# Kernel optimization log

Hardware: AMD Instinct MI355X
Metric: run time of the kernel (lower is better)

The kernel has to match this reference:

```python
import jax, jax.numpy as jnp
import numpy as np

B, N, C = 2, 120000, 80
K = 300            # fixed NMS candidate pad per class (>> expected ~150 above threshold)
MAX_DET = 100      # max_detections_per_images
SCORE_THRES = 0.99875
NMS_THRES = 0.5
MIN_SIZE = 1e-3    # remove_small_boxes min_size
BBOX_CLIP = float(np.log(1000.0 / 16.0))  # standard decode clamp on dw, dh


def _decode(deltas, anchors):
    # activ_2_bbox: standard anchor-delta decode (xyxy anchors)
    wa = anchors[:, 2] - anchors[:, 0]
    ha = anchors[:, 3] - anchors[:, 1]
    cxa = anchors[:, 0] + 0.5 * wa
    cya = anchors[:, 1] + 0.5 * ha
    dx, dy = deltas[:, 0], deltas[:, 1]
    dw = jnp.minimum(deltas[:, 2], BBOX_CLIP)
    dh = jnp.minimum(deltas[:, 3], BBOX_CLIP)
    cx = dx * wa + cxa
    cy = dy * ha + cya
    w = jnp.exp(dw) * wa
    h = jnp.exp(dh) * ha
    return jnp.stack([cx - 0.5 * w, cy - 0.5 * h, cx + 0.5 * w, cy + 0.5 * h], axis=-1)


def _pairwise_iou(b):
    area = (b[:, 2] - b[:, 0]) * (b[:, 3] - b[:, 1])
    lt = jnp.maximum(b[:, None, :2], b[None, :, :2])
    rb = jnp.minimum(b[:, None, 2:], b[None, :, 2:])
    wh = jnp.clip(rb - lt, 0.0)
    inter = wh[..., 0] * wh[..., 1]
    return inter / (area[:, None] + area[None, :] - inter + 1e-9)


def _nms_keep(boxes, valid):
    # boxes sorted by descending score; greedy suppression over K candidates
    iou = jax.lax.stop_gradient(_pairwise_iou(boxes))  # masks only -> no grad path
    idx = jnp.arange(boxes.shape[0])
    def body(keep, i):
        suppress = keep[i] & (iou[i] > NMS_THRES) & (idx > i)
        return keep & ~suppress, None
    keep, _ = jax.lax.scan(body, valid, idx)
    return keep


def _per_image(box_pred, cls_pred, anchors, H, W):
    boxes = _decode(box_pred, anchors)
    boxes = jnp.stack([
        jnp.clip(boxes[:, 0], 0.0, W), jnp.clip(boxes[:, 1], 0.0, H),
        jnp.clip(boxes[:, 2], 0.0, W), jnp.clip(boxes[:, 3], 0.0, H)], axis=-1)
    big = ((boxes[:, 2] - boxes[:, 0]) >= MIN_SIZE) & ((boxes[:, 3] - boxes[:, 1]) >= MIN_SIZE)

    def class_step(valid, c):
        # faithful to the original: the validity set carries over across classes
        sc = cls_pred[:, c]
        v = valid & big & (sc > SCORE_THRES)
        ms = jnp.where(v, sc, -jnp.inf)
        sk, idx = jax.lax.top_k(ms, K)            # sorted desc, fixed-size pad
        vk = sk > -jnp.inf
        bk = boxes[idx]                            # [K,4]
        keep = _nms_keep(bk, vk)
        keep = keep & ((jnp.cumsum(keep) - 1) < MAX_DET)  # keep[:max_det]
        new_valid = jnp.zeros_like(valid).at[idx].set(keep)
        bk = jnp.where(keep[:, None], bk, 0.0)
        sk = jnp.where(keep, sk, 0.0)
        return new_valid, (bk, sk, keep)

    _, (bks, sks, keeps) = jax.lax.scan(class_step, jnp.ones(boxes.shape[0], bool), jnp.arange(C))
    out5 = jnp.concatenate([bks, sks[..., None]], axis=-1).reshape(C * K, 5)
    labels = jnp.broadcast_to(jnp.arange(C, dtype=jnp.int32)[:, None], (C, K)).reshape(C * K)
    return out5, labels, keeps.reshape(C * K)


def setup_inputs() -> dict:
    key = jax.random.key(0)
    k1, k2, k3, k4, k5 = jax.random.split(key, 5)
    H, W = 800, 1216
    box_preds = 0.2 * jax.random.normal(k1, (B, N, 4), jnp.float32)
    cls_preds = jax.random.uniform(k2, (B, N, C), dtype=jnp.float32)
    cx = jax.random.uniform(k3, (N,), dtype=jnp.float32) * W
    cy = jax.random.uniform(k4, (N,), dtype=jnp.float32) * H
    wh = 16.0 + 240.0 * jax.random.uniform(k5, (N, 2), dtype=jnp.float32)
    anchors = jnp.stack([cx - 0.5 * wh[:, 0], cy - 0.5 * wh[:, 1],
                         cx + 0.5 * wh[:, 0], cy + 0.5 * wh[:, 1]], axis=-1)
    return {"box_preds": box_preds, "cls_preds": cls_preds, "anchors": anchors,
            "image_h": H, "image_w": W}


def reference(box_preds, cls_preds, anchors, image_h, image_w):
    H = jnp.float32(image_h)
    W = jnp.float32(image_w)
    out5, labels, keep = jax.vmap(lambda bp, cp: _per_image(bp, cp, anchors, H, W))(box_preds, cls_preds)
    # out5: [B, C*K, 5] (x1,y1,x2,y2,score), zero-padded where keep is False
    return out5, labels, keep
```

## Files before the change

### kernel.cpp

```cpp
#include <hip/hip_runtime.h>
#include <stdint.h>

#define B_ 2
#define N_ 120000
#define C_ 80
#define K_ 300
#define MAXDET 100
#define CAP 1024
#define KTOP 300
#define NW 5
#define NB 235
#define TPB 256
#define SLOTS 32

__device__ __constant__ float SCORE_THRES_F = 0.99875f;
__device__ __constant__ float NMS_THRES_F   = 0.5f;
__device__ __constant__ float MIN_SIZE_F    = 0.001f;
__device__ __constant__ float BBOX_CLIP_F   = 4.135166556742356f;

__global__ __launch_bounds__(TPB) void filter_init(
    const float* __restrict__ boxp, const float* __restrict__ clsp,
    const float* __restrict__ anch, const int* __restrict__ ih,
    const int* __restrict__ iw, int* __restrict__ cnt,
    int* __restrict__ g_idx, float* __restrict__ g_sc,
    float4* __restrict__ g_bx, float* __restrict__ out) {
#pragma clang fp contract(off)
    __shared__ int lcnt[2];
    const int blk = blockIdx.x;
    const int ltid = threadIdx.x;
    const int NT  = NB * TPB;
    const int tid = blk * TPB + ltid;
    if (ltid < 2) lcnt[ltid] = 0;

    const int BN = B_ * N_;
    float s[4]; int t4[4];
#pragma unroll
    for (int k = 0; k < 4; ++k) {
        int t = tid + k * NT;
        t4[k] = t;
        s[k] = (t < BN) ? clsp[(size_t)t * C_] : 0.f;
    }

    const int CK  = C_ * K_;
    const int L0  = B_ * CK * 5;
    const int L1  = L0 + B_ * CK;
    const int TOT = L1 + B_ * CK;
    for (int i = tid; i < TOT; i += NT) {
        float v = 0.f;
        if (i >= L0 && i < L1) { int r = i - L0; v = (float)((r % CK) / K_); }
        out[i] = v;
    }
    __syncthreads();

#pragma unroll
    for (int k = 0; k < 4; ++k) {
        int t = t4[k];
        if (t < BN && s[k] > SCORE_THRES_F) {
            int b = t / N_, n = t - b * N_;
            float W = (float)iw[0], H = (float)ih[0];
            float4 d = *(const float4*)(boxp + (size_t)t * 4);
            float4 a = *(const float4*)(anch + (size_t)n * 4);
            float wa = a.z - a.x, ha = a.w - a.y;
            float cxa = a.x + 0.5f * wa, cya = a.y + 0.5f * ha;
            float dw = fminf(d.z, BBOX_CLIP_F), dh = fminf(d.w, BBOX_CLIP_F);
            float cx = d.x * wa + cxa, cy = d.y * ha + cya;
            float w = expf(dw) * wa, h = expf(dh) * ha;
            float x1 = cx - 0.5f * w, y1 = cy - 0.5f * h;
            float x2 = cx + 0.5f * w, y2 = cy + 0.5f * h;
            x1 = fminf(fmaxf(x1, 0.f), W);
            y1 = fminf(fmaxf(y1, 0.f), H);
            x2 = fminf(fmaxf(x2, 0.f), W);
            y2 = fminf(fmaxf(y2, 0.f), H);
            if ((x2 - x1 >= MIN_SIZE_F) && (y2 - y1 >= MIN_SIZE_F)) {
                int p = atomicAdd(&lcnt[b], 1);
                if (p < SLOTS) {
                    int q = (b * NB + blk) * SLOTS + p;
                    g_idx[q] = n;
                    g_sc[q]  = s[k];
                    g_bx[q]  = make_float4(x1, y1, x2, y2);
                }
            }
        }
    }
    __syncthreads();
    if (ltid < 2) cnt[ltid * NB + blk] = min(lcnt[ltid], SLOTS);
}

__global__ __launch_bounds__(TPB) void seq_nms(const float* __restrict__ clsp,
                                               const int* __restrict__ cnt,
                                               const int* __restrict__ g_idx,
                                               const float* __restrict__ g_sc,
                                               const float4* __restrict__ g_bx,
                                               float* __restrict__ out) {
#pragma clang fp contract(off)
    const int b   = blockIdx.x;
    const int tid = threadIdx.x;
    const int BS  = blockDim.x;

    __shared__ __align__(16) float s_sc[CAP];
    __shared__ __align__(16) int   s_id[CAP];
    __shared__ float4 s_bx[CAP];
    __shared__ float  o_sc[KTOP];
    __shared__ int    o_id[KTOP];
    __shared__ float  o_ar[KTOP];
    __shared__ float  o_nsc[KTOP];
    __shared__ float4 o_bx[KTOP];
    __shared__ unsigned long long suppW[KTOP * NW];
    __shared__ unsigned long long keepm[NW];
    __shared__ int s_cnt, s_nk, s_m;
    __shared__ int wsum[4];
    __shared__ int    n_id[MAXDET];
    __shared__ float  n_sc[MAXDET];
    __shared__ float4 n_bx[MAXDET];

    if (tid == 0) s_nk = 0;
    const size_t CK = (size_t)C_ * K_;

    for (int c = 0; c < C_; ++c) {
        if (c > 0 && s_nk == 0) break;
        if (tid == 0) s_cnt = 0;
        __syncthreads();

        int m_in;
        if (c == 0) {
            int lane = tid & 63, wvi = tid >> 6;
            int v = (tid < NB) ? cnt[b * NB + tid] : 0;
            int x = v;
            for (int d = 1; d < 64; d <<= 1) {
                int y = __shfl_up(x, d);
                if (lane >= d) x += y;
            }
            if (lane == 63) wsum[wvi] = x;
            __syncthreads();
            int offbase = 0;
            for (int w = 0; w < wvi; ++w) offbase += wsum[w];
            if (tid == BS - 1) s_m = offbase + x;
            int excl = offbase + x - v;
            for (int j = 0; j < v; ++j) {
                int dst = excl + j;
                if (dst < CAP) {
                    int src = (b * NB + tid) * SLOTS + j;
                    s_sc[dst] = g_sc[src];
                    s_id[dst] = g_idx[src];
                    s_bx[dst] = g_bx[src];
                }
            }
            __syncthreads();
            m_in = min(s_m, CAP);
        } else {
            int nk = s_nk;
            for (int t = tid; t < nk; t += BS) {
                float sv = n_sc[t];
                if (sv > SCORE_THRES_F) {
                    int p = atomicAdd(&s_cnt, 1);
                    s_sc[p] = sv; s_id[p] = n_id[t]; s_bx[p] = n_bx[t];
                }
            }
            __syncthreads();
            m_in = s_cnt;
        }
        int m = min(m_in, KTOP);
        if (m == 0) {
            if (tid == 0) s_nk = 0;
            __syncthreads();
            continue;
        }

        for (int i = tid; i < m_in; i += BS) {
            float si = s_sc[i]; int di = s_id[i]; float4 bx = s_bx[i];
            float ns = 0.f;
            if (c + 1 < C_) ns = clsp[((size_t)(b * N_) + di) * C_ + (c + 1)];
            int rank = 0;
            int m4 = m_in & ~3;
            for (int j = 0; j < m4; j += 4) {
                float4 sj = *(const float4*)&s_sc[j];
                int4   dj = *(const int4*)&s_id[j];
                rank += (sj.x > si) || (sj.x == si && dj.x < di);
                rank += (sj.y > si) || (sj.y == si && dj.y < di);
                rank += (sj.z > si) || (sj.z == si && dj.z < di);
                rank += (sj.w > si) || (sj.w == si && dj.w < di);
            }
            for (int j = m4; j < m_in; ++j) {
                float sj = s_sc[j];
                rank += (sj > si) || (sj == si && s_id[j] < di);
            }
            if (rank < KTOP) {
                o_sc[rank] = si; o_id[rank] = di; o_bx[rank] = bx;
                o_ar[rank] = (bx.z - bx.x) * (bx.w - bx.y);
                o_nsc[rank] = ns;
            }
        }
        __syncthreads();

        for (int i = tid; i < m; i += BS) {
            float4 bi = o_bx[i]; float ai = o_ar[i];
            for (int w = 0; w < NW; ++w) {
                unsigned long long msk = 0ull;
                int jlo = max(i + 1, w * 64);
                int jhi = min(m, w * 64 + 64);
#pragma unroll 4
                for (int j = jlo; j < jhi; ++j) {
                    float4 bj = o_bx[j];
                    float lx = fmaxf(bi.x, bj.x), ly = fmaxf(bi.y, bj.y);
                    float rx = fminf(bi.z, bj.z), ry = fminf(bi.w, bj.w);
                    float ww = fmaxf(rx - lx, 0.f), hh = fmaxf(ry - ly, 0.f);
                    float inter = ww * hh;
                    float arj = (bj.z - bj.x) * (bj.w - bj.y);
                    float iou = inter / (ai + arj - inter + 1e-9f);
                    if (iou > NMS_THRES_F) msk |= 1ull << (j & 63);
                }
                suppW[i * NW + w] = msk;
            }
        }
        __syncthreads();

        if (tid < 64) {
            int lane = tid;
            unsigned long long km = 0ull;
            if (lane < NW) {
                int nb = m - lane * 64;
                if (nb >= 64) km = ~0ull;
                else if (nb > 0) km = (1ull << nb) - 1ull;
            }
            unsigned long long srow = (lane < NW) ? suppW[lane] : 0ull;
            for (int i = 0; i < m; ++i) {
                unsigned long long nxt =
                    (lane < NW && i + 1 < m) ? suppW[(i + 1) * NW + lane] : 0ull;
                unsigned long long wv = __shfl(km, i >> 6);
                if ((wv >> (i & 63)) & 1ull) km &= ~srow;
                srow = nxt;
            }
            unsigned long long w0 = __shfl(km, 0), w1 = __shfl(km, 1),
                               w2 = __shfl(km, 2), w3 = __shfl(km, 3),
                               w4 = __shfl(km, 4);
            if (lane == 0) {
                unsigned long long arr[NW] = {w0, w1, w2, w3, w4};
                int cnt2 = 0;
                for (int w = 0; w < NW; ++w) {
                    unsigned long long x = arr[w];
                    if (cnt2 >= MAXDET) { arr[w] = 0ull; continue; }
                    int pc = __popcll(x);
                    if (cnt2 + pc > MAXDET) {
                        int need = MAXDET - cnt2;
                        unsigned long long y = x;
                        for (int k2 = 0; k2 < need; ++k2) y &= y - 1ull;
                        arr[w] = x ^ y;
                        cnt2 = MAXDET;
                    } else cnt2 += pc;
                }
                int tot = 0;
                for (int w = 0; w < NW; ++w) { keepm[w] = arr[w]; tot += __popcll(arr[w]); }
                s_nk = tot;
            }
        }
        __syncthreads();

        for (int r = tid; r < m; r += BS) {
            unsigned long long wv = keepm[r >> 6];
            if ((wv >> (r & 63)) & 1ull) {
                int pos = __popcll(wv & ((1ull << (r & 63)) - 1ull));
                for (int w = 0; w < (r >> 6); ++w) pos += __popcll(keepm[w]);
                size_t row = (size_t)b * CK + (size_t)c * K_ + r;
                float4 bx = o_bx[r];
                float* o5 = out + row * 5;
                o5[0] = bx.x; o5[1] = bx.y; o5[2] = bx.z; o5[3] = bx.w;
                o5[4] = o_sc[r];
                out[(size_t)B_ * CK * 6 + row] = 1.0f;
                n_id[pos] = o_id[r];
                n_bx[pos] = bx;
                n_sc[pos] = o_nsc[r];
            }
        }
    }
}

extern "C" void kernel_launch(void* const* d_in, const int* in_sizes, int n_in,
                              void* d_out, int out_size, void* d_ws, size_t ws_size,
                              hipStream_t stream) {
    const float* boxp = (const float*)d_in[0];
    const float* clsp = (const float*)d_in[1];
    const float* anch = (const float*)d_in[2];
    const int*   ih   = (const int*)d_in[3];
    const int*   iw   = (const int*)d_in[4];
    float* out = (float*)d_out;

    int*    cnt   = (int*)d_ws;
    int*    g_idx = (int*)((char*)d_ws + 4096);
    float*  g_sc  = (float*)((char*)d_ws + 4096 + (size_t)B_ * NB * SLOTS * 4);
    float4* g_bx  = (float4*)((char*)d_ws + 4096 + (size_t)B_ * NB * SLOTS * 8);

    filter_init<<<NB, TPB, 0, stream>>>(boxp, clsp, anch, ih, iw,
                                        cnt, g_idx, g_sc, g_bx, out);
    seq_nms<<<B_, TPB, 0, stream>>>(clsp, cnt, g_idx, g_sc, g_bx, out);
}
```

Baseline: 149.8 us.

## Fuse filter and NMS into one cooperative kernel; bit-skip greedy NMS scan

Merges the filter/decode kernel and the per-image sequential NMS kernel into a single cooperative launch with a grid-wide sync, removing one kernel launch and the inter-kernel gap. The greedy suppression loop now preloads the suppression rows into registers and walks only the surviving candidate bits with ctz and readlane, instead of iterating over every candidate with shuffles. The cooperative launch needs all 237 blocks resident at once, and a grid sync has its own cost. The fused kernel also carries the large NMS shared-memory footprint in every block, which may limit occupancy during the filter phase.

```diff
diff --git a/kernel.cpp b/kernel.cpp
--- a/kernel.cpp
+++ b/kernel.cpp
@@ -1,5 +1,8 @@
 #include <hip/hip_runtime.h>
+#include <hip/hip_cooperative_groups.h>
 #include <stdint.h>
+
+namespace cg = cooperative_groups;
 
 #define B_ 2
 #define N_ 120000
@@ -18,85 +21,23 @@
 __device__ __constant__ float MIN_SIZE_F    = 0.001f;
 __device__ __constant__ float BBOX_CLIP_F   = 4.135166556742356f;
 
-__global__ __launch_bounds__(TPB) void filter_init(
+__device__ __forceinline__ unsigned long long rl64(unsigned long long v, int lane) {
+    unsigned lo = (unsigned)__builtin_amdgcn_readlane((int)(unsigned)(v & 0xffffffffull), lane);
+    unsigned hi = (unsigned)__builtin_amdgcn_readlane((int)(unsigned)(v >> 32), lane);
+    return ((unsigned long long)hi << 32) | lo;
+}
+
+__global__ __launch_bounds__(TPB) void retina_fused(
     const float* __restrict__ boxp, const float* __restrict__ clsp,
     const float* __restrict__ anch, const int* __restrict__ ih,
     const int* __restrict__ iw, int* __restrict__ cnt,
     int* __restrict__ g_idx, float* __restrict__ g_sc,
     float4* __restrict__ g_bx, float* __restrict__ out) {
 #pragma clang fp contract(off)
+    const int blk  = blockIdx.x;
+    const int ltid = threadIdx.x;
+
     __shared__ int lcnt[2];
-    const int blk = blockIdx.x;
-    const int ltid = threadIdx.x;
-    const int NT  = NB * TPB;
-    const int tid = blk * TPB + ltid;
-    if (ltid < 2) lcnt[ltid] = 0;
-
-    const int BN = B_ * N_;
-    float s[4]; int t4[4];
-#pragma unroll
-    for (int k = 0; k < 4; ++k) {
-        int t = tid + k * NT;
-        t4[k] = t;
-        s[k] = (t < BN) ? clsp[(size_t)t * C_] : 0.f;
-    }
-
-    const int CK  = C_ * K_;
-    const int L0  = B_ * CK * 5;
-    const int L1  = L0 + B_ * CK;
-    const int TOT = L1 + B_ * CK;
-    for (int i = tid; i < TOT; i += NT) {
-        float v = 0.f;
-        if (i >= L0 && i < L1) { int r = i - L0; v = (float)((r % CK) / K_); }
-        out[i] = v;
-    }
-    __syncthreads();
-
-#pragma unroll
-    for (int k = 0; k < 4; ++k) {
-        int t = t4[k];
-        if (t < BN && s[k] > SCORE_THRES_F) {
-            int b = t / N_, n = t - b * N_;
-            float W = (float)iw[0], H = (float)ih[0];
-            float4 d = *(const float4*)(boxp + (size_t)t * 4);
-            float4 a = *(const float4*)(anch + (size_t)n * 4);
-            float wa = a.z - a.x, ha = a.w - a.y;
-            float cxa = a.x + 0.5f * wa, cya = a.y + 0.5f * ha;
-            float dw = fminf(d.z, BBOX_CLIP_F), dh = fminf(d.w, BBOX_CLIP_F);
-            float cx = d.x * wa + cxa, cy = d.y * ha + cya;
-            float w = expf(dw) * wa, h = expf(dh) * ha;
-            float x1 = cx - 0.5f * w, y1 = cy - 0.5f * h;
-            float x2 = cx + 0.5f * w, y2 = cy + 0.5f * h;
-            x1 = fminf(fmaxf(x1, 0.f), W);
-            y1 = fminf(fmaxf(y1, 0.f), H);
-            x2 = fminf(fmaxf(x2, 0.f), W);
-            y2 = fminf(fmaxf(y2, 0.f), H);
-            if ((x2 - x1 >= MIN_SIZE_F) && (y2 - y1 >= MIN_SIZE_F)) {
-                int p = atomicAdd(&lcnt[b], 1);
-                if (p < SLOTS) {
-                    int q = (b * NB + blk) * SLOTS + p;
-                    g_idx[q] = n;
-                    g_sc[q]  = s[k];
-                    g_bx[q]  = make_float4(x1, y1, x2, y2);
-                }
-            }
-        }
-    }
-    __syncthreads();
-    if (ltid < 2) cnt[ltid * NB + blk] = min(lcnt[ltid], SLOTS);
-}
-
-__global__ __launch_bounds__(TPB) void seq_nms(const float* __restrict__ clsp,
-                                               const int* __restrict__ cnt,
-                                               const int* __restrict__ g_idx,
-                                               const float* __restrict__ g_sc,
-                                               const float4* __restrict__ g_bx,
-                                               float* __restrict__ out) {
-#pragma clang fp contract(off)
-    const int b   = blockIdx.x;
-    const int tid = threadIdx.x;
-    const int BS  = blockDim.x;
-
     __shared__ __align__(16) float s_sc[CAP];
     __shared__ __align__(16) int   s_id[CAP];
     __shared__ float4 s_bx[CAP];
@@ -112,6 +53,72 @@
     __shared__ int    n_id[MAXDET];
     __shared__ float  n_sc[MAXDET];
     __shared__ float4 n_bx[MAXDET];
+
+    if (blk < NB) {
+        const int NT  = NB * TPB;
+        const int tid = blk * TPB + ltid;
+        if (ltid < 2) lcnt[ltid] = 0;
+
+        const int BN = B_ * N_;
+        float s[4]; int t4[4];
+#pragma unroll
+        for (int k = 0; k < 4; ++k) {
+            int t = tid + k * NT;
+            t4[k] = t;
+            s[k] = (t < BN) ? clsp[(size_t)t * C_] : 0.f;
+        }
+
+        const int CK  = C_ * K_;
+        const int L0  = B_ * CK * 5;
+        const int L1  = L0 + B_ * CK;
+        const int TOT = L1 + B_ * CK;
+        for (int i = tid; i < TOT; i += NT) {
+            float v = 0.f;
+            if (i >= L0 && i < L1) { int r = i - L0; v = (float)((r % CK) / K_); }
+            out[i] = v;
+        }
+        __syncthreads();
+
+#pragma unroll
+        for (int k = 0; k < 4; ++k) {
+            int t = t4[k];
+            if (t < BN && s[k] > SCORE_THRES_F) {
+                int b = t / N_, n = t - b * N_;
+                float W = (float)iw[0], H = (float)ih[0];
+                float4 d = *(const float4*)(boxp + (size_t)t * 4);
+                float4 a = *(const float4*)(anch + (size_t)n * 4);
+                float wa = a.z - a.x, ha = a.w - a.y;
+                float cxa = a.x + 0.5f * wa, cya = a.y + 0.5f * ha;
+                float dw = fminf(d.z, BBOX_CLIP_F), dh = fminf(d.w, BBOX_CLIP_F);
+                float cx = d.x * wa + cxa, cy = d.y * ha + cya;
+                float w = expf(dw) * wa, h = expf(dh) * ha;
+                float x1 = cx - 0.5f * w, y1 = cy - 0.5f * h;
+                float x2 = cx + 0.5f * w, y2 = cy + 0.5f * h;
+                x1 = fminf(fmaxf(x1, 0.f), W);
+                y1 = fminf(fmaxf(y1, 0.f), H);
+                x2 = fminf(fmaxf(x2, 0.f), W);
+                y2 = fminf(fmaxf(y2, 0.f), H);
+                if ((x2 - x1 >= MIN_SIZE_F) && (y2 - y1 >= MIN_SIZE_F)) {
+                    int p = atomicAdd(&lcnt[b], 1);
+                    if (p < SLOTS) {
+                        int q = (b * NB + blk) * SLOTS + p;
+                        g_idx[q] = n;
+                        g_sc[q]  = s[k];
+                        g_bx[q]  = make_float4(x1, y1, x2, y2);
+                    }
+                }
+            }
+        }
+        __syncthreads();
+        if (ltid < 2) cnt[ltid * NB + blk] = min(lcnt[ltid], SLOTS);
+    }
+
+    cg::this_grid().sync();
+    if (blk < NB) return;
+
+    const int b   = blk - NB;
+    const int tid = ltid;
+    const int BS  = TPB;
 
     if (tid == 0) s_nk = 0;
     const size_t CK = (size_t)C_ * K_;
@@ -215,42 +222,50 @@
         __syncthreads();
 
         if (tid < 64) {
-            int lane = tid;
-            unsigned long long km = 0ull;
-            if (lane < NW) {
-                int nb = m - lane * 64;
-                if (nb >= 64) km = ~0ull;
-                else if (nb > 0) km = (1ull << nb) - 1ull;
-            }
-            unsigned long long srow = (lane < NW) ? suppW[lane] : 0ull;
-            for (int i = 0; i < m; ++i) {
-                unsigned long long nxt =
-                    (lane < NW && i + 1 < m) ? suppW[(i + 1) * NW + lane] : 0ull;
-                unsigned long long wv = __shfl(km, i >> 6);
-                if ((wv >> (i & 63)) & 1ull) km &= ~srow;
-                srow = nxt;
-            }
-            unsigned long long w0 = __shfl(km, 0), w1 = __shfl(km, 1),
-                               w2 = __shfl(km, 2), w3 = __shfl(km, 3),
-                               w4 = __shfl(km, 4);
+            const int lane = tid;
+            unsigned long long row[NW][NW];
+#pragma unroll
+            for (int g = 0; g < NW; ++g) {
+                int i = g * 64 + lane;
+#pragma unroll
+                for (int w = 0; w < NW; ++w)
+                    row[g][w] = (w >= g && i < m) ? suppW[i * NW + w] : 0ull;
+            }
+            unsigned long long km[NW];
+#pragma unroll
+            for (int w = 0; w < NW; ++w) {
+                int nb2 = m - w * 64;
+                km[w] = (nb2 >= 64) ? ~0ull : (nb2 > 0 ? ((1ull << nb2) - 1ull) : 0ull);
+            }
+#pragma unroll
+            for (int g = 0; g < NW; ++g) {
+                unsigned long long pend = km[g];
+                while (pend) {
+                    int t = __builtin_ctzll(pend);
+#pragma unroll
+                    for (int w = 0; w < NW; ++w)
+                        if (w >= g) km[w] &= ~rl64(row[g][w], t);
+                    pend = (t >= 63) ? 0ull : (km[g] & (~0ull << (t + 1)));
+                }
+            }
+            int cnt2 = 0;
+#pragma unroll
+            for (int w = 0; w < NW; ++w) {
+                unsigned long long x = km[w];
+                if (cnt2 >= MAXDET) { km[w] = 0ull; continue; }
+                int pc = __popcll(x);
+                if (cnt2 + pc > MAXDET) {
+                    int need = MAXDET - cnt2;
+                    unsigned long long y = x;
+                    for (int k2 = 0; k2 < need; ++k2) y &= y - 1ull;
+                    km[w] = x ^ y;
+                    cnt2 = MAXDET;
+                } else cnt2 += pc;
+            }
             if (lane == 0) {
-                unsigned long long arr[NW] = {w0, w1, w2, w3, w4};
-                int cnt2 = 0;
-                for (int w = 0; w < NW; ++w) {
-                    unsigned long long x = arr[w];
-                    if (cnt2 >= MAXDET) { arr[w] = 0ull; continue; }
-                    int pc = __popcll(x);
-                    if (cnt2 + pc > MAXDET) {
-                        int need = MAXDET - cnt2;
-                        unsigned long long y = x;
-                        for (int k2 = 0; k2 < need; ++k2) y &= y - 1ull;
-                        arr[w] = x ^ y;
-                        cnt2 = MAXDET;
-                    } else cnt2 += pc;
-                }
-                int tot = 0;
-                for (int w = 0; w < NW; ++w) { keepm[w] = arr[w]; tot += __popcll(arr[w]); }
-                s_nk = tot;
+#pragma unroll
+                for (int w = 0; w < NW; ++w) keepm[w] = km[w];
+                s_nk = cnt2;
             }
         }
         __syncthreads();
@@ -260,12 +275,12 @@
             if ((wv >> (r & 63)) & 1ull) {
                 int pos = __popcll(wv & ((1ull << (r & 63)) - 1ull));
                 for (int w = 0; w < (r >> 6); ++w) pos += __popcll(keepm[w]);
-                size_t row = (size_t)b * CK + (size_t)c * K_ + r;
+                size_t row_ = (size_t)b * CK + (size_t)c * K_ + r;
                 float4 bx = o_bx[r];
-                float* o5 = out + row * 5;
+                float* o5 = out + row_ * 5;
                 o5[0] = bx.x; o5[1] = bx.y; o5[2] = bx.z; o5[3] = bx.w;
                 o5[4] = o_sc[r];
-                out[(size_t)B_ * CK * 6 + row] = 1.0f;
+                out[(size_t)B_ * CK * 6 + row_] = 1.0f;
                 n_id[pos] = o_id[r];
                 n_bx[pos] = bx;
                 n_sc[pos] = o_nsc[r];
@@ -282,14 +297,16 @@
     const float* anch = (const float*)d_in[2];
     const int*   ih   = (const int*)d_in[3];
     const int*   iw   = (const int*)d_in[4];
-    float* out = (float*)d_out;
+    float* outp = (float*)d_out;
 
     int*    cnt   = (int*)d_ws;
     int*    g_idx = (int*)((char*)d_ws + 4096);
     float*  g_sc  = (float*)((char*)d_ws + 4096 + (size_t)B_ * NB * SLOTS * 4);
     float4* g_bx  = (float4*)((char*)d_ws + 4096 + (size_t)B_ * NB * SLOTS * 8);
 
-    filter_init<<<NB, TPB, 0, stream>>>(boxp, clsp, anch, ih, iw,
-                                        cnt, g_idx, g_sc, g_bx, out);
-    seq_nms<<<B_, TPB, 0, stream>>>(clsp, cnt, g_idx, g_sc, g_bx, out);
+    void* args[] = {(void*)&boxp, (void*)&clsp, (void*)&anch, (void*)&ih,
+                    (void*)&iw, (void*)&cnt, (void*)&g_idx, (void*)&g_sc,
+                    (void*)&g_bx, (void*)&outp};
+    hipLaunchCooperativeKernel((void*)retina_fused, dim3(NB + B_), dim3(TPB),
+                               args, 0, stream);
 }
```

New measurement: 193.6 us. 29.3% more time.
